# Optimization experiments

Hardware: AMD Instinct MI355X
Metric: run time of the kernel (lower is better)

Reference implementation:

```python
import jax, jax.numpy as jnp
import numpy as np

B, T, D, H = 64, 512, 512, 1024


def setup_inputs() -> dict:
    key = jax.random.key(0)
    ks = jax.random.split(key, 13)
    s = 1.0 / np.sqrt(H)  # keep gates in a sane range
    inp = {"x": jax.random.normal(ks[0], (B, T, D), dtype=jnp.float32)}
    wshapes = {
        "W_zx": (D, H), "W_zh": (H, H),
        "W_rx": (D, H), "W_rh": (H, H),
        "W_nx": (D, H), "W_nh": (H, H),
    }
    i = 1
    for name, shape in wshapes.items():
        inp[name] = jax.random.normal(ks[i], shape, dtype=jnp.float32) * s
        i += 1
    for name in ["b_zx", "b_zh", "b_rx", "b_rh", "b_nx", "b_nh"]:
        inp[name] = jax.random.normal(ks[i], (1, H), dtype=jnp.float32) * s
        i += 1
    return inp


def reference(x, W_zx, W_zh, W_rx, W_rh, W_nx, W_nh,
              b_zx, b_zh, b_rx, b_rh, b_nx, b_nh):
    # Precompute all input-side projections in 3 batched GEMMs: [B,T,H]
    xz = jnp.einsum('btd,dh->bth', x, W_zx) + b_zx
    xr = jnp.einsum('btd,dh->bth', x, W_rx) + b_rx
    xn = jnp.einsum('btd,dh->bth', x, W_nx) + b_nx

    def step(h, ins):
        xz_t, xr_t, xn_t = ins  # each [B,H]
        z = jax.nn.sigmoid(xz_t + h @ W_zh + b_zh)
        r = jax.nn.sigmoid(xr_t + h @ W_rh + b_rh)
        n = jnp.tanh(xn_t + r * (h @ W_nh + b_nh))
        h = (1.0 - z) * n + z * h
        return h, None

    h0 = jnp.zeros((x.shape[0], W_zh.shape[0]), dtype=x.dtype)
    # scan over time: inputs transposed to [T,B,H]
    h_final, _ = jax.lax.scan(
        step, h0,
        (xz.transpose(1, 0, 2), xr.transpose(1, 0, 2), xn.transpose(1, 0, 2)))
    return h_final
```

## Files before the change

### kernel.cpp

```cpp
#include <hip/hip_runtime.h>
#include <math.h>

#define T_STEPS 512
#define Bb 64
#define Dd 512
#define Hh 1024
#define NBLK 256

typedef __attribute__((ext_vector_type(8))) short short8;
typedef __attribute__((ext_vector_type(4))) float floatx4;
typedef __attribute__((ext_vector_type(4))) unsigned int uint4v;

__device__ __forceinline__ unsigned short f2bf(float f) {
    unsigned u = __float_as_uint(f);
    unsigned r = u + 0x7fffu + ((u >> 16) & 1u);
    return (unsigned short)(r >> 16);
}
__device__ __forceinline__ float bf2f(unsigned short h) {
    return __uint_as_float(((unsigned)h) << 16);
}
__device__ __forceinline__ float gru_h(float zs, float rs, float us, float vs,
                                       float bz, float br, float bu, float bv,
                                       float hprev) {
    float z = 1.f / (1.f + __expf(-(zs + bz)));
    float r = 1.f / (1.f + __expf(-(rs + br)));
    float n = 1.f - 2.f / (__expf(2.f * (us + bu + r * (vs + bv))) + 1.f);
    return (1.f - z) * n + z * hprev;
}
__device__ __forceinline__ short8 cvt8(float4 a, float4 b) {
    short8 s;
    s[0] = (short)f2bf(a.x); s[1] = (short)f2bf(a.y);
    s[2] = (short)f2bf(a.z); s[3] = (short)f2bf(a.w);
    s[4] = (short)f2bf(b.x); s[5] = (short)f2bf(b.y);
    s[6] = (short)f2bf(b.z); s[7] = (short)f2bf(b.w);
    return s;
}

__global__ __launch_bounds__(256) void build_wsw(
    const float* __restrict__ Wzx, const float* __restrict__ Wzh,
    const float* __restrict__ Wrx, const float* __restrict__ Wrh,
    const float* __restrict__ Wnx, const float* __restrict__ Wnh,
    unsigned short* __restrict__ wsw)
{
    int idx = blockIdx.x * 256 + threadIdx.x;
    int l = idx & 63;
    int rest = idx >> 6;
    int g = rest % 3; rest /= 3;
    int ks = rest % 48;
    int ct = rest / 48;
    if (ct >= 64) return;
    int k0 = ks * 32 + ((l >> 4) << 3);
    int n  = ct * 16 + (l & 15);
    const float* Wx = (g == 0) ? Wzx : (g == 1) ? Wrx : Wnx;
    const float* Wh = (g == 0) ? Wzh : (g == 1) ? Wrh : Wnh;
    const float* src = (k0 < Dd) ? (Wx + (size_t)k0 * Hh + n)
                                 : (Wh + (size_t)(k0 - Dd) * Hh + n);
    size_t base = ((((size_t)ct * 48 + ks) * 3 + g) * 2) * 512;
    unsigned short* hi = wsw + base + l * 8;
    unsigned short* lo = hi + 512;
    #pragma unroll
    for (int j = 0; j < 8; ++j) {
        float w = src[(size_t)j * Hh];
        unsigned short h16 = f2bf(w);
        hi[j] = h16;
        lo[j] = f2bf(w - bf2f(h16));
    }
}

#define WDECL(i) uint4v uzh##i, uzl##i, urh##i, url##i, unh##i, unl##i
#define WLOADA(i, ksv) do { \
    const unsigned short* wp = wsw + (size_t)(cb * 48 + (ksv)) * 3072 + lane * 8; \
    asm volatile("global_load_dwordx4 %0, %1, off" : "=&v"(uzh##i) : "v"(wp)        ); \
    asm volatile("global_load_dwordx4 %0, %1, off" : "=&v"(uzl##i) : "v"(wp + 512)  ); \
    asm volatile("global_load_dwordx4 %0, %1, off" : "=&v"(urh##i) : "v"(wp + 1024) ); \
    asm volatile("global_load_dwordx4 %0, %1, off" : "=&v"(url##i) : "v"(wp + 1536) ); \
    asm volatile("global_load_dwordx4 %0, %1, off" : "=&v"(unh##i) : "v"(wp + 2048) ); \
    asm volatile("global_load_dwordx4 %0, %1, off" : "=&v"(unl##i) : "v"(wp + 2560) ); \
} while (0)
#define WS(name) __builtin_bit_cast(short8, name)
#define XMFMA(i, av) do { \
    aZ  = __builtin_amdgcn_mfma_f32_16x16x32_bf16(av, WS(uzh##i), aZ,  0, 0, 0); \
    aZ  = __builtin_amdgcn_mfma_f32_16x16x32_bf16(av, WS(uzl##i), aZ,  0, 0, 0); \
    aR  = __builtin_amdgcn_mfma_f32_16x16x32_bf16(av, WS(urh##i), aR,  0, 0, 0); \
    aR  = __builtin_amdgcn_mfma_f32_16x16x32_bf16(av, WS(url##i), aR,  0, 0, 0); \
    aNx = __builtin_amdgcn_mfma_f32_16x16x32_bf16(av, WS(unh##i), aNx, 0, 0, 0); \
    aNx = __builtin_amdgcn_mfma_f32_16x16x32_bf16(av, WS(unl##i), aNx, 0, 0, 0); } while (0)
#define HMFMA(i, av) do { \
    aZ  = __builtin_amdgcn_mfma_f32_16x16x32_bf16(av, WS(uzh##i), aZ,  0, 0, 0); \
    aZ  = __builtin_amdgcn_mfma_f32_16x16x32_bf16(av, WS(uzl##i), aZ,  0, 0, 0); \
    aR  = __builtin_amdgcn_mfma_f32_16x16x32_bf16(av, WS(urh##i), aR,  0, 0, 0); \
    aR  = __builtin_amdgcn_mfma_f32_16x16x32_bf16(av, WS(url##i), aR,  0, 0, 0); \
    aNh = __builtin_amdgcn_mfma_f32_16x16x32_bf16(av, WS(unh##i), aNh, 0, 0, 0); \
    aNh = __builtin_amdgcn_mfma_f32_16x16x32_bf16(av, WS(unl##i), aNh, 0, 0, 0); } while (0)
#define LOADX(tt) do { const float* xp = xrow + (size_t)(tt) * Dd; \
    xf0 = *(const float4*)(xp);      xf1 = *(const float4*)(xp + 4); \
    xf2 = *(const float4*)(xp + 32); xf3 = *(const float4*)(xp + 36); } while (0)

__global__ __launch_bounds__(512, 2) void gru_persist(
    const float* __restrict__ x,
    const float* __restrict__ bzx, const float* __restrict__ bzh,
    const float* __restrict__ brx, const float* __restrict__ brh,
    const float* __restrict__ bnx, const float* __restrict__ bnh,
    const unsigned short* __restrict__ wsw,
    unsigned short* __restrict__ hbuf,
    unsigned* __restrict__ bar,
    float* __restrict__ out)
{
    __shared__ float part[8][4][64][4];

    const int tid  = threadIdx.x;
    const int lane = tid & 63;
    const int wave = tid >> 6;
    const int bx   = blockIdx.x;
    const int rb   = bx >> 6;
    const int cb   = bx & 63;
    unsigned* flags = bar + (rb << 10);

    const int R0   = rb << 4;
    const int orow = tid >> 4;
    const int ocol = tid & 15;
    const int gcol = (cb << 4) + ocol;
    const int pl   = ((orow & 12) << 2) | ocol;
    const int pq   = orow & 3;
    const float bz  = bzx[gcol] + bzh[gcol];
    const float brr = brx[gcol] + brh[gcol];
    const float bu  = bnx[gcol];
    const float bv  = bnh[gcol];
    float hprev = 0.f;

    const int arow  = lane & 15;
    const int acol8 = (lane >> 4) << 3;
    const float* xrow = x + (size_t)(R0 + arow) * (T_STEPS * Dd) + wave * 64 + acol8;

    WDECL(0); WDECL(1); WDECL(2); WDECL(3); WDECL(4); WDECL(5);
    WLOADA(0, wave * 2);      WLOADA(1, wave * 2 + 1);
    WLOADA(2, 16 + wave * 4); WLOADA(3, 17 + wave * 4);
    WLOADA(4, 18 + wave * 4); WLOADA(5, 19 + wave * 4);
    asm volatile("s_waitcnt vmcnt(0)" ::: "memory");
    __builtin_amdgcn_sched_barrier(0);

    float4 xf0, xf1, xf2, xf3;
    floatx4 aZ = {0.f,0.f,0.f,0.f}, aR = aZ, aNx = aZ;
    LOADX(0);
    {
        short8 xa0 = cvt8(xf0, xf1), xa1 = cvt8(xf2, xf3);
        XMFMA(0, xa0); XMFMA(1, xa1);
    }
    LOADX(1);

    for (int t = 0; t < T_STEPS; ++t) {
        if (t) {
            if (wave == 0) {
                const unsigned* fp = flags + (lane << 4);
                unsigned v;
                for (;;) {
                    asm volatile("global_load_dword %0, %1, off sc0 sc1\n\t"
                                 "s_waitcnt vmcnt(0)"
                                 : "=&v"(v) : "v"(fp) : "memory");
                    if (__all(v >= (unsigned)t)) break;
                    __builtin_amdgcn_s_sleep(1);
                }
            }
            __syncthreads();
        }

        const unsigned short* hrow = hbuf
            + ((size_t)((((t & 1) ^ 1) * Bb) + R0 + arow) << 10)
            + (wave << 7) + acol8;
        uint4v h0, h1, h2, h3;
        asm volatile("global_load_dwordx4 %0, %1, off sc0 sc1"            : "=&v"(h0) : "v"(hrow) : "memory");
        asm volatile("global_load_dwordx4 %0, %1, off offset:64 sc0 sc1"  : "=&v"(h1) : "v"(hrow) : "memory");
        asm volatile("global_load_dwordx4 %0, %1, off offset:128 sc0 sc1" : "=&v"(h2) : "v"(hrow) : "memory");
        asm volatile("global_load_dwordx4 %0, %1, off offset:192 sc0 sc1" : "=&v"(h3) : "v"(hrow) : "memory");
        asm volatile("s_waitcnt vmcnt(0)" ::: "memory");
        __builtin_amdgcn_sched_barrier(0);

        floatx4 aNh = {0.f,0.f,0.f,0.f};
        {
            short8 a0 = __builtin_bit_cast(short8, h0);
            short8 a1 = __builtin_bit_cast(short8, h1);
            short8 a2 = __builtin_bit_cast(short8, h2);
            short8 a3 = __builtin_bit_cast(short8, h3);
            HMFMA(2, a0); HMFMA(3, a1); HMFMA(4, a2); HMFMA(5, a3);
        }

        *(floatx4*)&part[wave][0][lane][0] = aZ;
        *(floatx4*)&part[wave][1][lane][0] = aR;
        *(floatx4*)&part[wave][2][lane][0] = aNx;
        *(floatx4*)&part[wave][3][lane][0] = aNh;
        __syncthreads();

        if (tid < 256) {
            float zs = 0.f, rs = 0.f, us = 0.f, vs = 0.f;
            #pragma unroll
            for (int w = 0; w < 8; ++w) {
                zs += part[w][0][pl][pq];
                rs += part[w][1][pl][pq];
                us += part[w][2][pl][pq];
                vs += part[w][3][pl][pq];
            }
            float h = gru_h(zs, rs, us, vs, bz, brr, bu, bv, hprev);
            hprev = h;
            unsigned hv = (unsigned)f2bf(h);
            const unsigned short* hptr = hbuf
                + ((size_t)((t & 1) * Bb + R0 + orow) << 10) + gcol;
            asm volatile("global_store_short %0, %1, off sc0 sc1"
                         :: "v"(hptr), "v"(hv) : "memory");
        }
        asm volatile("s_waitcnt vmcnt(0)" ::: "memory");
        __syncthreads();

        if (tid == 0) {
            unsigned fv = (unsigned)(t + 1);
            asm volatile("global_store_dword %0, %1, off sc0 sc1"
                         :: "v"(flags + (cb << 4)), "v"(fv) : "memory");
        }

        if (t + 1 < T_STEPS) {
            floatx4 z4 = {0.f,0.f,0.f,0.f};
            aZ = z4; aR = z4; aNx = z4;
            short8 xa0 = cvt8(xf0, xf1), xa1 = cvt8(xf2, xf3);
            XMFMA(0, xa0); XMFMA(1, xa1);
            if (t + 2 < T_STEPS) LOADX(t + 2);
            __builtin_amdgcn_sched_barrier(0);
        }
    }

    if (tid < 256)
        out[(size_t)(R0 + orow) * Hh + gcol] = hprev;
}

extern "C" void kernel_launch(void* const* d_in, const int* in_sizes, int n_in,
                              void* d_out, int out_size, void* d_ws, size_t ws_size,
                              hipStream_t stream) {
    const float* x   = (const float*)d_in[0];
    const float* Wzx = (const float*)d_in[1];
    const float* Wzh = (const float*)d_in[2];
    const float* Wrx = (const float*)d_in[3];
    const float* Wrh = (const float*)d_in[4];
    const float* Wnx = (const float*)d_in[5];
    const float* Wnh = (const float*)d_in[6];
    const float* bzx = (const float*)d_in[7];
    const float* bzh = (const float*)d_in[8];
    const float* brx = (const float*)d_in[9];
    const float* brh = (const float*)d_in[10];
    const float* bnx = (const float*)d_in[11];
    const float* bnh = (const float*)d_in[12];

    unsigned char* ws = (unsigned char*)d_ws;
    unsigned* bar = (unsigned*)ws;
    unsigned short* hbuf = (unsigned short*)(ws + 16384);
    unsigned short* wsw  = (unsigned short*)(ws + 16384 + 262144);

    hipMemsetAsync(bar, 0, 16384, stream);
    hipMemsetAsync(hbuf, 0, (size_t)2 * Bb * Hh * sizeof(unsigned short), stream);

    build_wsw<<<2304, 256, 0, stream>>>(Wzx, Wzh, Wrx, Wrh, Wnx, Wnh, wsw);

    gru_persist<<<NBLK, 512, 0, stream>>>(x, bzx, bzh, brx, brh, bnx, bnh,
                                          wsw, hbuf, bar, (float*)d_out);
}
```

Before: 2.076 ms.

## Replace block-wide flag wait with per-wave chunked polling and staged h stores

Each wave now polls only the producer flags covering its own slice of h and issues each 16-byte h load as soon as its 4 producer blocks have signalled. This replaces the wave-0 spin followed by a __syncthreads. New h values are gathered in LDS and written by wave 0 as dwordx2 stores instead of per-thread short stores. The flag store is moved after the next step's x-projection MFMAs so that work overlaps the store drain. It adds polling traffic, since all 8 waves now spin on global flags, and risks memory-ordering subtleties, because the LDS hshare buffer is reused across steps without a barrier before the next write.

```diff
diff --git a/kernel.cpp b/kernel.cpp
--- a/kernel.cpp
+++ b/kernel.cpp
@@ -10,6 +10,7 @@
 typedef __attribute__((ext_vector_type(8))) short short8;
 typedef __attribute__((ext_vector_type(4))) float floatx4;
 typedef __attribute__((ext_vector_type(4))) unsigned int uint4v;
+typedef __attribute__((ext_vector_type(2))) unsigned int uint2v;
 
 __device__ __forceinline__ unsigned short f2bf(float f) {
     unsigned u = __float_as_uint(f);
@@ -107,6 +108,7 @@
     float* __restrict__ out)
 {
     __shared__ float part[8][4][64][4];
+    __shared__ unsigned short hshare[16][16];
 
     const int tid  = threadIdx.x;
     const int lane = tid & 63;
@@ -132,6 +134,11 @@
     const int acol8 = (lane >> 4) << 3;
     const float* xrow = x + (size_t)(R0 + arow) * (T_STEPS * Dd) + wave * 64 + acol8;
 
+    const unsigned* fp = flags + (((wave << 3) | (lane & 7)) << 4);
+    const int prow = lane >> 2;
+    const int pcol = (lane & 3) << 2;
+    unsigned short* pdst0 = hbuf + ((size_t)(R0 + prow) << 10) + (cb << 4) + pcol;
+
     WDECL(0); WDECL(1); WDECL(2); WDECL(3); WDECL(4); WDECL(5);
     WLOADA(0, wave * 2);      WLOADA(1, wave * 2 + 1);
     WLOADA(2, 16 + wave * 4); WLOADA(3, 17 + wave * 4);
@@ -149,29 +156,38 @@
     LOADX(1);
 
     for (int t = 0; t < T_STEPS; ++t) {
-        if (t) {
-            if (wave == 0) {
-                const unsigned* fp = flags + (lane << 4);
-                unsigned v;
-                for (;;) {
-                    asm volatile("global_load_dword %0, %1, off sc0 sc1\n\t"
-                                 "s_waitcnt vmcnt(0)"
-                                 : "=&v"(v) : "v"(fp) : "memory");
-                    if (__all(v >= (unsigned)t)) break;
-                    __builtin_amdgcn_s_sleep(1);
-                }
-            }
-            __syncthreads();
-        }
-
         const unsigned short* hrow = hbuf
             + ((size_t)((((t & 1) ^ 1) * Bb) + R0 + arow) << 10)
             + (wave << 7) + acol8;
         uint4v h0, h1, h2, h3;
-        asm volatile("global_load_dwordx4 %0, %1, off sc0 sc1"            : "=&v"(h0) : "v"(hrow) : "memory");
-        asm volatile("global_load_dwordx4 %0, %1, off offset:64 sc0 sc1"  : "=&v"(h1) : "v"(hrow) : "memory");
-        asm volatile("global_load_dwordx4 %0, %1, off offset:128 sc0 sc1" : "=&v"(h2) : "v"(hrow) : "memory");
-        asm volatile("global_load_dwordx4 %0, %1, off offset:192 sc0 sc1" : "=&v"(h3) : "v"(hrow) : "memory");
+        if (t) {
+            unsigned v; int j = 0;
+            for (;;) {
+                asm volatile("global_load_dword %0, %1, off sc0 sc1\n\t"
+                             "s_waitcnt vmcnt(0)"
+                             : "=&v"(v) : "v"(fp) : "memory");
+                unsigned long long m = __ballot(v >= (unsigned)t);
+                if (j == 0 && (m & 0x0303030303030303ull) == 0x0303030303030303ull) {
+                    asm volatile("global_load_dwordx4 %0, %1, off sc0 sc1"
+                                 : "=&v"(h0) : "v"(hrow) : "memory"); j = 1; }
+                if (j == 1 && (m & 0x0C0C0C0C0C0C0C0Cull) == 0x0C0C0C0C0C0C0C0Cull) {
+                    asm volatile("global_load_dwordx4 %0, %1, off offset:64 sc0 sc1"
+                                 : "=&v"(h1) : "v"(hrow) : "memory"); j = 2; }
+                if (j == 2 && (m & 0x3030303030303030ull) == 0x3030303030303030ull) {
+                    asm volatile("global_load_dwordx4 %0, %1, off offset:128 sc0 sc1"
+                                 : "=&v"(h2) : "v"(hrow) : "memory"); j = 3; }
+                if (j == 3 && (m & 0xC0C0C0C0C0C0C0C0ull) == 0xC0C0C0C0C0C0C0C0ull) {
+                    asm volatile("global_load_dwordx4 %0, %1, off offset:192 sc0 sc1"
+                                 : "=&v"(h3) : "v"(hrow) : "memory"); j = 4; }
+                if (j == 4) break;
+                __builtin_amdgcn_s_sleep(1);
+            }
+        } else {
+            asm volatile("global_load_dwordx4 %0, %1, off sc0 sc1"            : "=&v"(h0) : "v"(hrow) : "memory");
+            asm volatile("global_load_dwordx4 %0, %1, off offset:64 sc0 sc1"  : "=&v"(h1) : "v"(hrow) : "memory");
+            asm volatile("global_load_dwordx4 %0, %1, off offset:128 sc0 sc1" : "=&v"(h2) : "v"(hrow) : "memory");
+            asm volatile("global_load_dwordx4 %0, %1, off offset:192 sc0 sc1" : "=&v"(h3) : "v"(hrow) : "memory");
+        }
         asm volatile("s_waitcnt vmcnt(0)" ::: "memory");
         __builtin_amdgcn_sched_barrier(0);
 
@@ -201,19 +217,15 @@
             }
             float h = gru_h(zs, rs, us, vs, bz, brr, bu, bv, hprev);
             hprev = h;
-            unsigned hv = (unsigned)f2bf(h);
-            const unsigned short* hptr = hbuf
-                + ((size_t)((t & 1) * Bb + R0 + orow) << 10) + gcol;
-            asm volatile("global_store_short %0, %1, off sc0 sc1"
-                         :: "v"(hptr), "v"(hv) : "memory");
-        }
-        asm volatile("s_waitcnt vmcnt(0)" ::: "memory");
+            hshare[orow][ocol] = f2bf(h);
+        }
         __syncthreads();
 
-        if (tid == 0) {
-            unsigned fv = (unsigned)(t + 1);
-            asm volatile("global_store_dword %0, %1, off sc0 sc1"
-                         :: "v"(flags + (cb << 4)), "v"(fv) : "memory");
+        if (wave == 0) {
+            uint2v hv2 = *(const uint2v*)&hshare[prow][pcol];
+            const unsigned short* hptr = pdst0 + ((size_t)(t & 1) * Bb << 10);
+            asm volatile("global_store_dwordx2 %0, %1, off sc0 sc1"
+                         :: "v"(hptr), "v"(hv2) : "memory");
         }
 
         if (t + 1 < T_STEPS) {
@@ -223,6 +235,15 @@
             XMFMA(0, xa0); XMFMA(1, xa1);
             if (t + 2 < T_STEPS) LOADX(t + 2);
             __builtin_amdgcn_sched_barrier(0);
+        }
+
+        if (wave == 0) {
+            asm volatile("s_waitcnt vmcnt(0)" ::: "memory");
+            if (lane == 0) {
+                unsigned fv = (unsigned)(t + 1);
+                asm volatile("global_store_dword %0, %1, off sc0 sc1"
+                             :: "v"(flags + (cb << 4)), "v"(fv) : "memory");
+            }
         }
     }
 
```

Result: slower. 2.311 ms (+11.3%).

## Replace flag barrier with tagged hidden-state words polled directly

Applied to the files above, without the earlier changes.

Drops the separate per-block flag array and its spin-wait barrier. Each hidden value is now stored as a 32-bit word with the bf16 value in the high half and the step tag in the low half. Consumers poll the h-buffer itself until every tag they need matches, then unpack the bf16 halves. This removes one global round trip per step (the flag store, the flag poll and the store-drain wait) in exchange for reading twice as many bytes for h and doing extra unpacking work.

```diff
diff --git a/kernel.cpp b/kernel.cpp
--- a/kernel.cpp
+++ b/kernel.cpp
@@ -95,6 +95,11 @@
 #define LOADX(tt) do { const float* xp = xrow + (size_t)(tt) * Dd; \
     xf0 = *(const float4*)(xp);      xf1 = *(const float4*)(xp + 4); \
     xf2 = *(const float4*)(xp + 32); xf3 = *(const float4*)(xp + 36); } while (0)
+#define PACKF(dst, lo, hi) do { \
+    dst[0] = (short)(lo[0] >> 16); dst[1] = (short)(lo[1] >> 16); \
+    dst[2] = (short)(lo[2] >> 16); dst[3] = (short)(lo[3] >> 16); \
+    dst[4] = (short)(hi[0] >> 16); dst[5] = (short)(hi[1] >> 16); \
+    dst[6] = (short)(hi[2] >> 16); dst[7] = (short)(hi[3] >> 16); } while (0)
 
 __global__ __launch_bounds__(512, 2) void gru_persist(
     const float* __restrict__ x,
@@ -102,11 +107,11 @@
     const float* __restrict__ brx, const float* __restrict__ brh,
     const float* __restrict__ bnx, const float* __restrict__ bnh,
     const unsigned short* __restrict__ wsw,
-    unsigned short* __restrict__ hbuf,
-    unsigned* __restrict__ bar,
+    unsigned* __restrict__ hbuf,
     float* __restrict__ out)
 {
     __shared__ float part[8][4][64][4];
+    __shared__ unsigned hshare[16][16];
 
     const int tid  = threadIdx.x;
     const int lane = tid & 63;
@@ -114,7 +119,6 @@
     const int bx   = blockIdx.x;
     const int rb   = bx >> 6;
     const int cb   = bx & 63;
-    unsigned* flags = bar + (rb << 10);
 
     const int R0   = rb << 4;
     const int orow = tid >> 4;
@@ -132,6 +136,9 @@
     const int acol8 = (lane >> 4) << 3;
     const float* xrow = x + (size_t)(R0 + arow) * (T_STEPS * Dd) + wave * 64 + acol8;
 
+    const unsigned* qbase = hbuf + ((size_t)(R0 + arow) << 10) + (wave << 7) + acol8;
+    unsigned* pbase = hbuf + ((size_t)(R0 + (lane >> 2)) << 10) + (cb << 4) + ((lane & 3) << 2);
+
     WDECL(0); WDECL(1); WDECL(2); WDECL(3); WDECL(4); WDECL(5);
     WLOADA(0, wave * 2);      WLOADA(1, wave * 2 + 1);
     WLOADA(2, 16 + wave * 4); WLOADA(3, 17 + wave * 4);
@@ -149,38 +156,33 @@
     LOADX(1);
 
     for (int t = 0; t < T_STEPS; ++t) {
-        if (t) {
-            if (wave == 0) {
-                const unsigned* fp = flags + (lane << 4);
-                unsigned v;
-                for (;;) {
-                    asm volatile("global_load_dword %0, %1, off sc0 sc1\n\t"
-                                 "s_waitcnt vmcnt(0)"
-                                 : "=&v"(v) : "v"(fp) : "memory");
-                    if (__all(v >= (unsigned)t)) break;
-                    __builtin_amdgcn_s_sleep(1);
-                }
-            }
-            __syncthreads();
-        }
-
-        const unsigned short* hrow = hbuf
-            + ((size_t)((((t & 1) ^ 1) * Bb) + R0 + arow) << 10)
-            + (wave << 7) + acol8;
-        uint4v h0, h1, h2, h3;
-        asm volatile("global_load_dwordx4 %0, %1, off sc0 sc1"            : "=&v"(h0) : "v"(hrow) : "memory");
-        asm volatile("global_load_dwordx4 %0, %1, off offset:64 sc0 sc1"  : "=&v"(h1) : "v"(hrow) : "memory");
-        asm volatile("global_load_dwordx4 %0, %1, off offset:128 sc0 sc1" : "=&v"(h2) : "v"(hrow) : "memory");
-        asm volatile("global_load_dwordx4 %0, %1, off offset:192 sc0 sc1" : "=&v"(h3) : "v"(hrow) : "memory");
-        asm volatile("s_waitcnt vmcnt(0)" ::: "memory");
+        const unsigned* hq = qbase + (((size_t)((t & 1) ^ 1)) << 16);
+        const unsigned tagv = (unsigned)t;
+        uint4v c0, c1, c2, c3, c4, c5, c6, c7;
+        for (;;) {
+            asm volatile("global_load_dwordx4 %0, %1, off sc0 sc1"            : "=&v"(c0) : "v"(hq) : "memory");
+            asm volatile("global_load_dwordx4 %0, %1, off offset:16 sc0 sc1"  : "=&v"(c1) : "v"(hq) : "memory");
+            asm volatile("global_load_dwordx4 %0, %1, off offset:128 sc0 sc1" : "=&v"(c2) : "v"(hq) : "memory");
+            asm volatile("global_load_dwordx4 %0, %1, off offset:144 sc0 sc1" : "=&v"(c3) : "v"(hq) : "memory");
+            asm volatile("global_load_dwordx4 %0, %1, off offset:256 sc0 sc1" : "=&v"(c4) : "v"(hq) : "memory");
+            asm volatile("global_load_dwordx4 %0, %1, off offset:272 sc0 sc1" : "=&v"(c5) : "v"(hq) : "memory");
+            asm volatile("global_load_dwordx4 %0, %1, off offset:384 sc0 sc1" : "=&v"(c6) : "v"(hq) : "memory");
+            asm volatile("global_load_dwordx4 %0, %1, off offset:400 sc0 sc1" : "=&v"(c7) : "v"(hq) : "memory");
+            asm volatile("s_waitcnt vmcnt(0)" ::: "memory");
+            bool ok = ((c0[0] & 0xffffu) == tagv) & ((c1[0] & 0xffffu) == tagv)
+                    & ((c2[0] & 0xffffu) == tagv) & ((c3[0] & 0xffffu) == tagv)
+                    & ((c4[0] & 0xffffu) == tagv) & ((c5[0] & 0xffffu) == tagv)
+                    & ((c6[0] & 0xffffu) == tagv) & ((c7[0] & 0xffffu) == tagv);
+            if (__all(ok)) break;
+            __builtin_amdgcn_s_sleep(1);
+        }
         __builtin_amdgcn_sched_barrier(0);
 
         floatx4 aNh = {0.f,0.f,0.f,0.f};
         {
-            short8 a0 = __builtin_bit_cast(short8, h0);
-            short8 a1 = __builtin_bit_cast(short8, h1);
-            short8 a2 = __builtin_bit_cast(short8, h2);
-            short8 a3 = __builtin_bit_cast(short8, h3);
+            short8 a0, a1, a2, a3;
+            PACKF(a0, c0, c1); PACKF(a1, c2, c3);
+            PACKF(a2, c4, c5); PACKF(a3, c6, c7);
             HMFMA(2, a0); HMFMA(3, a1); HMFMA(4, a2); HMFMA(5, a3);
         }
 
@@ -201,19 +203,15 @@
             }
             float h = gru_h(zs, rs, us, vs, bz, brr, bu, bv, hprev);
             hprev = h;
-            unsigned hv = (unsigned)f2bf(h);
-            const unsigned short* hptr = hbuf
-                + ((size_t)((t & 1) * Bb + R0 + orow) << 10) + gcol;
-            asm volatile("global_store_short %0, %1, off sc0 sc1"
-                         :: "v"(hptr), "v"(hv) : "memory");
-        }
-        asm volatile("s_waitcnt vmcnt(0)" ::: "memory");
+            hshare[orow][ocol] = (((unsigned)f2bf(h)) << 16) | (unsigned)(t + 1);
+        }
         __syncthreads();
 
-        if (tid == 0) {
-            unsigned fv = (unsigned)(t + 1);
-            asm volatile("global_store_dword %0, %1, off sc0 sc1"
-                         :: "v"(flags + (cb << 4)), "v"(fv) : "memory");
+        if (wave == 0) {
+            uint4v hv = *(const uint4v*)&hshare[lane >> 2][(lane & 3) << 2];
+            unsigned* pdst = pbase + (((size_t)(t & 1)) << 16);
+            asm volatile("global_store_dwordx4 %0, %1, off sc0 sc1"
+                         :: "v"(pdst), "v"(hv) : "memory");
         }
 
         if (t + 1 < T_STEPS) {
@@ -248,15 +246,13 @@
     const float* bnh = (const float*)d_in[12];
 
     unsigned char* ws = (unsigned char*)d_ws;
-    unsigned* bar = (unsigned*)ws;
-    unsigned short* hbuf = (unsigned short*)(ws + 16384);
-    unsigned short* wsw  = (unsigned short*)(ws + 16384 + 262144);
-
-    hipMemsetAsync(bar, 0, 16384, stream);
-    hipMemsetAsync(hbuf, 0, (size_t)2 * Bb * Hh * sizeof(unsigned short), stream);
+    unsigned* hbuf = (unsigned*)ws;
+    unsigned short* wsw = (unsigned short*)(ws + 524288);
+
+    hipMemsetAsync(hbuf, 0, (size_t)2 * Bb * Hh * sizeof(unsigned), stream);
 
     build_wsw<<<2304, 256, 0, stream>>>(Wzx, Wzh, Wrx, Wrh, Wnx, Wnh, wsw);
 
     gru_persist<<<NBLK, 512, 0, stream>>>(x, bzx, bzh, brx, brh, bnx, bnh,
-                                          wsw, hbuf, bar, (float*)d_out);
-}
+                                          wsw, hbuf, (float*)d_out);
+}
```

Result: slower. 3.109 ms (+49.7%).
